# Optimization experiments

Hardware: AMD Instinct MI355X
Metric: run time of the kernel (lower is better)

The kernel has to match this reference:

```python
import jax, jax.numpy as jnp
import numpy as np

B, N, DIM = 8, 1024, 512
HEADS, DIM_HEAD = 8, 64
INNER = HEADS * DIM_HEAD  # 512
SCALE = DIM_HEAD ** -0.5
EPS = 1e-5


def setup_inputs() -> dict:
    key = jax.random.key(0)
    k = jax.random.split(key, 6)
    x = jax.random.normal(k[0], (B, N, DIM), dtype=jnp.float32)
    gamma = jnp.ones((DIM,), dtype=jnp.float32)
    beta = jnp.zeros((DIM,), dtype=jnp.float32)
    # Linear weights stored as (in, out) so y = x @ W (equivalent to torch x @ W.T)
    W_qk = jax.random.normal(k[1], (DIM, 2 * INNER), dtype=jnp.float32) * (DIM ** -0.5)
    W_v = jax.random.normal(k[2], (DIM, INNER), dtype=jnp.float32) * (DIM ** -0.5)
    W_out = jax.random.normal(k[3], (INNER, DIM), dtype=jnp.float32) * (INNER ** -0.5)
    return {"x": x, "gamma": gamma, "beta": beta, "W_qk": W_qk, "W_v": W_v, "W_out": W_out}


def _layernorm(x, gamma, beta):
    mu = jnp.mean(x, axis=-1, keepdims=True)
    var = jnp.mean(jnp.square(x - mu), axis=-1, keepdims=True)
    return (x - mu) * jax.lax.rsqrt(var + EPS) * gamma + beta


def reference(x, gamma, beta, W_qk, W_v, W_out):
    xn = _layernorm(x, gamma, beta)                       # [B,N,D]
    v = xn @ W_v                                          # [B,N,INNER]
    qk = xn @ W_qk                                        # [B,N,2*INNER]
    q, k = jnp.split(qk, 2, axis=-1)
    # b n (h d) -> b h n d
    q = q.reshape(B, N, HEADS, DIM_HEAD).transpose(0, 2, 1, 3)
    k = k.reshape(B, N, HEADS, DIM_HEAD).transpose(0, 2, 1, 3)
    vh = v.reshape(B, N, HEADS, DIM_HEAD).transpose(0, 2, 1, 3)
    dots = jnp.einsum('bhnd,bhmd->bhnm', q, k) * SCALE    # [B,H,N,N]
    attn = jax.nn.softmax(dots, axis=-1)
    out = jnp.einsum('bhnm,bhmd->bhnd', attn, vh)         # [B,H,N,d]
    out = out.transpose(0, 2, 1, 3).reshape(B, N, INNER)  # b h n d -> b n (h d)
    return out @ W_out                                    # [B,N,DIM]
```

## Files before the change

### kernel.cpp

```cpp
#include <hip/hip_runtime.h>

#define TOK 8192
#define DMODEL 512
#define SEQ 1024
#define NH 8
#define DH 64

typedef _Float16 half8 __attribute__((ext_vector_type(8)));
typedef _Float16 half4v __attribute__((ext_vector_type(4)));
typedef float floatx4 __attribute__((ext_vector_type(4)));
typedef unsigned int uint2v __attribute__((ext_vector_type(2)));

__device__ __forceinline__ void gll16(const void* g, void* l) {
  __builtin_amdgcn_global_load_lds(
      (const __attribute__((address_space(1))) void*)g,
      (__attribute__((address_space(3))) void*)l, 16, 0, 0);
}

__device__ __forceinline__ unsigned pk16(float a, float b) {
  auto v = __builtin_amdgcn_cvt_pkrtz(a, b);
  return __builtin_bit_cast(unsigned, v);
}

__global__ __launch_bounds__(256) void prep_kernel(
    const float* __restrict__ x, const float* __restrict__ gamma,
    const float* __restrict__ beta, _Float16* __restrict__ xn,
    const float* __restrict__ Wqk, const float* __restrict__ Wv,
    const float* __restrict__ Wo, _Float16* __restrict__ WqkvT,
    _Float16* __restrict__ WoutT) {
  __shared__ float t[32][33];
  const int bid = blockIdx.x;
  if (bid < 2048) {
    const int row = bid * 4 + (threadIdx.x >> 6);
    const int tt = threadIdx.x & 63;
    const float* xr = x + (size_t)row * DMODEL;
    const float4 a = *(const float4*)(xr + tt * 4);
    const float4 b = *(const float4*)(xr + 256 + tt * 4);
    float s  = a.x + a.y + a.z + a.w + b.x + b.y + b.z + b.w;
    float ss = a.x*a.x + a.y*a.y + a.z*a.z + a.w*a.w
             + b.x*b.x + b.y*b.y + b.z*b.z + b.w*b.w;
    #pragma unroll
    for (int m = 1; m < 64; m <<= 1) {
      s  += __shfl_xor(s, m);
      ss += __shfl_xor(ss, m);
    }
    const float mean = s * (1.0f / DMODEL);
    const float var  = ss * (1.0f / DMODEL) - mean * mean;
    const float inv  = rsqrtf(var + 1e-5f);
    const float4 g0  = *(const float4*)(gamma + tt * 4);
    const float4 g1  = *(const float4*)(gamma + 256 + tt * 4);
    const float4 be0 = *(const float4*)(beta + tt * 4);
    const float4 be1 = *(const float4*)(beta + 256 + tt * 4);
    half4v o0, o1;
    o0[0] = (_Float16)((a.x - mean) * inv * g0.x + be0.x);
    o0[1] = (_Float16)((a.y - mean) * inv * g0.y + be0.y);
    o0[2] = (_Float16)((a.z - mean) * inv * g0.z + be0.z);
    o0[3] = (_Float16)((a.w - mean) * inv * g0.w + be0.w);
    o1[0] = (_Float16)((b.x - mean) * inv * g1.x + be1.x);
    o1[1] = (_Float16)((b.y - mean) * inv * g1.y + be1.y);
    o1[2] = (_Float16)((b.z - mean) * inv * g1.z + be1.z);
    o1[3] = (_Float16)((b.w - mean) * inv * g1.w + be1.w);
    _Float16* outr = xn + (size_t)row * DMODEL;
    *(half4v*)(outr + tt * 4) = o0;
    *(half4v*)(outr + 256 + tt * 4) = o1;
  } else {
    const int r = bid - 2048;
    const int z = r >> 9;
    const int rem = r & 511;
    const float* W;
    _Float16* dst;
    int N, rowoff;
    if (z == 0)      { W = Wqk; dst = WqkvT; N = 1024; rowoff = 0; }
    else if (z == 1) { W = Wv;  dst = WqkvT; N = 512;  rowoff = 1024; }
    else             { W = Wo;  dst = WoutT; N = 512;  rowoff = 0; }
    const int n0 = (rem & 31) * 32;
    if (n0 >= N) return;
    const int k0 = (rem >> 5) * 32;
    const int tx = threadIdx.x & 31, ty = threadIdx.x >> 5;
    #pragma unroll
    for (int j = 0; j < 4; ++j)
      t[ty + j * 8][tx] = W[(size_t)(k0 + ty + j * 8) * N + n0 + tx];
    __syncthreads();
    #pragma unroll
    for (int j = 0; j < 4; ++j)
      dst[(size_t)(rowoff + n0 + ty + j * 8) * 512 + k0 + tx] =
          (_Float16)t[tx][ty + j * 8];
  }
}

__global__ __launch_bounds__(256) void hgemm_qkv(
    const _Float16* __restrict__ A, const _Float16* __restrict__ Bt,
    _Float16* __restrict__ Q, _Float16* __restrict__ V, int K) {
  __shared__ char smem[49152];
  const int tid = threadIdx.x;
  const int bm = blockIdx.x, bn = blockIdx.y;
  const int wv = tid >> 6, lane = tid & 63;
  const int l15 = lane & 15, g = lane >> 4;
  const int wr = wv >> 1, wc = wv & 1;
  const _Float16* Ab = A + (size_t)(bm * 128) * K;
  const _Float16* Bb = Bt + (size_t)(bn * 128) * K;
  const int lrow = lane >> 2;
  const int lchk = (lane & 3) * 16;
  const int ssw = lchk ^ (((lrow >> 1) & 3) << 4);

  #define HG_STAGE(buf, kt)                                                   \
    _Pragma("unroll")                                                         \
    for (int i = 0; i < 2; ++i) {                                             \
      const int rbase = wv * 16 + i * 64;                                     \
      gll16((const char*)(Ab + (size_t)(rbase + lrow) * K + (kt)) + ssw,      \
            smem + (buf) * 16384 + rbase * 64);                               \
      gll16((const char*)(Bb + (size_t)(rbase + lrow) * K + (kt)) + ssw,      \
            smem + (buf) * 16384 + 8192 + rbase * 64);                        \
    }

  floatx4 acc[4][4] = {};
  HG_STAGE(0, 0);
  HG_STAGE(1, 32);
  int cur = 0;
  const int nit = K >> 5;
  for (int it = 0; it < nit; ++it) {
    if (it < nit - 2) asm volatile("s_waitcnt vmcnt(4)" ::: "memory");
    else              asm volatile("s_waitcnt vmcnt(0)" ::: "memory");
    __builtin_amdgcn_s_barrier();
    asm volatile("" ::: "memory");
    const int nxt = cur + 2 >= 3 ? cur - 1 : cur + 2;
    if (it + 2 < nit) { HG_STAGE(nxt, (it + 2) * 32); }
    const char* sb = smem + cur * 16384;
    half8 af[4], bf[4];
    #pragma unroll
    for (int mt = 0; mt < 4; ++mt) {
      const int row = wr * 64 + mt * 16 + l15;
      af[mt] = *(const half8*)(sb + row * 64 +
                               ((g * 16) ^ (((row >> 1) & 3) << 4)));
    }
    #pragma unroll
    for (int nt = 0; nt < 4; ++nt) {
      const int row = wc * 64 + nt * 16 + l15;
      bf[nt] = *(const half8*)(sb + 8192 + row * 64 +
                               ((g * 16) ^ (((row >> 1) & 3) << 4)));
    }
    __builtin_amdgcn_s_setprio(1);
    #pragma unroll
    for (int mt = 0; mt < 4; ++mt)
      #pragma unroll
      for (int nt = 0; nt < 4; ++nt)
        acc[mt][nt] = __builtin_amdgcn_mfma_f32_16x16x32_f16(
            af[mt], bf[nt], acc[mt][nt], 0, 0, 0);
    __builtin_amdgcn_s_setprio(0);
    cur = cur + 1 >= 3 ? 0 : cur + 1;
  }
  #undef HG_STAGE
  const int m0 = bm * 128 + wr * 64;
  const int n0 = bn * 128 + wc * 64;
  #pragma unroll
  for (int mt = 0; mt < 4; ++mt) {
    const int mrow = m0 + mt * 16 + 4 * g;
    const int b = mrow >> 10, tok = mrow & 1023;
    #pragma unroll
    for (int nt = 0; nt < 4; ++nt) {
      const int n = n0 + nt * 16 + l15;
      if (n < 1024) {
        #pragma unroll
        for (int r = 0; r < 4; ++r)
          Q[(size_t)(mrow + r) * 1024 + n] = (_Float16)acc[mt][nt][r];
      } else {
        const int cv = n - 1024;
        half4v hv;
        #pragma unroll
        for (int r = 0; r < 4; ++r) hv[r] = (_Float16)acc[mt][nt][r];
        *(half4v*)(V + ((size_t)((b * 8 + (cv >> 6)) * 64 + (cv & 63)) << 10) + tok) = hv;
      }
    }
  }
}

__global__ __launch_bounds__(512) void hgemm_out(
    const _Float16* __restrict__ A, const _Float16* __restrict__ Bt,
    float* __restrict__ C) {
  __shared__ char smem[49152];
  const int tid = threadIdx.x;
  const int bm = blockIdx.x, bn = blockIdx.y;
  const int wv = tid >> 6, lane = tid & 63;
  const int l15 = lane & 15, g = lane >> 4;
  const int wr = wv >> 2, wc = wv & 3;
  const _Float16* Ab = A + (size_t)(bm * 128) * 512;
  const _Float16* Bb = Bt + (size_t)(bn * 128) * 512;
  const int lrow = lane >> 2;
  const int lchk = (lane & 3) * 16;
  const int ssw = lchk ^ (((lrow >> 1) & 3) << 4);

  #define OUT_STAGE(buf, kt)                                                  \
    {                                                                         \
      gll16((const char*)(Ab + (size_t)(wv * 16 + lrow) * 512 + (kt)) + ssw,  \
            smem + (buf) * 16384 + wv * 16 * 64);                             \
      gll16((const char*)(Bb + (size_t)(wv * 16 + lrow) * 512 + (kt)) + ssw,  \
            smem + (buf) * 16384 + 8192 + wv * 16 * 64);                      \
    }

  floatx4 acc[4][2] = {};
  OUT_STAGE(0, 0);
  OUT_STAGE(1, 32);
  int cur = 0;
  for (int it = 0; it < 16; ++it) {
    if (it < 14) asm volatile("s_waitcnt vmcnt(2)" ::: "memory");
    else         asm volatile("s_waitcnt vmcnt(0)" ::: "memory");
    __builtin_amdgcn_s_barrier();
    asm volatile("" ::: "memory");
    const int nxt = cur + 2 >= 3 ? cur - 1 : cur + 2;
    if (it + 2 < 16) { OUT_STAGE(nxt, (it + 2) * 32); }
    const char* sb = smem + cur * 16384;
    half8 af[4], bf[2];
    #pragma unroll
    for (int mt = 0; mt < 4; ++mt) {
      const int row = wr * 64 + mt * 16 + l15;
      af[mt] = *(const half8*)(sb + row * 64 +
                               ((g * 16) ^ (((row >> 1) & 3) << 4)));
    }
    #pragma unroll
    for (int nt = 0; nt < 2; ++nt) {
      const int row = wc * 32 + nt * 16 + l15;
      bf[nt] = *(const half8*)(sb + 8192 + row * 64 +
                               ((g * 16) ^ (((row >> 1) & 3) << 4)));
    }
    __builtin_amdgcn_s_setprio(1);
    #pragma unroll
    for (int mt = 0; mt < 4; ++mt)
      #pragma unroll
      for (int nt = 0; nt < 2; ++nt)
        acc[mt][nt] = __builtin_amdgcn_mfma_f32_16x16x32_f16(
            af[mt], bf[nt], acc[mt][nt], 0, 0, 0);
    __builtin_amdgcn_s_setprio(0);
    cur = cur + 1 >= 3 ? 0 : cur + 1;
  }
  #undef OUT_STAGE
  const int m0 = bm * 128 + wr * 64;
  const int n0 = bn * 128 + wc * 32;
  #pragma unroll
  for (int mt = 0; mt < 4; ++mt)
    #pragma unroll
    for (int nt = 0; nt < 2; ++nt) {
      const int n = n0 + nt * 16 + l15;
      #pragma unroll
      for (int r = 0; r < 4; ++r)
        C[(size_t)(m0 + mt * 16 + 4 * g + r) * 512 + n] = acc[mt][nt][r];
    }
}

#define QSC 0.18033688f
#define MOFF 5.7707801f

__global__ __launch_bounds__(512) void flash16_kernel(
    const _Float16* __restrict__ qkh, const _Float16* __restrict__ vt,
    _Float16* __restrict__ ao) {
  __shared__ char smem[65536];
  const int bh = blockIdx.x;
  const int qt = blockIdx.y;
  const int b = bh >> 3, h = bh & 7;
  const int tid = threadIdx.x;
  const int wv = tid >> 6, lane = tid & 63;
  const int l15 = lane & 15, g = lane >> 4;
  const int swz = (l15 & 7) << 4;
  const int qrow0 = b * SEQ + qt * 128;

  half8 qf[2];
  {
    const _Float16* qp = qkh + (size_t)(qrow0 + wv * 16 + l15) * 1024 + h * DH;
    qf[0] = *(const half8*)(qp + g * 8);
    qf[1] = *(const half8*)(qp + g * 8 + 32);
    qf[0] *= (_Float16)QSC;
    qf[1] *= (_Float16)QSC;
  }

  float lsum = 0.f;
  floatx4 oacc[4] = {};
  floatx4 minit;
  minit[0] = -MOFF; minit[1] = -MOFF; minit[2] = -MOFF; minit[3] = -MOFF;

  const int lrow = lane >> 3;
  const int lchk = (lane & 7) * 16;
  const int ssw = lchk ^ (lrow << 4);
  const _Float16* kbase = qkh + 512 + h * DH;
  const _Float16* vbase = vt + (size_t)bh * 64 * 1024;
  char* pb = smem + 49152 + wv * 2048 + l15 * 128;

  #define FL_STAGE(buf, kt)                                                   \
    {                                                                         \
      const int krow = b * SEQ + (kt) * 64 + wv * 8 + lrow;                   \
      gll16((const char*)(kbase + (size_t)krow * 1024) + ssw,                 \
            smem + (buf) * 16384 + wv * 1024);                                \
      gll16((const char*)(vbase + (size_t)(wv * 8 + lrow) * 1024 +            \
                          (kt) * 64) + ssw,                                   \
            smem + (buf) * 16384 + 8192 + wv * 1024);                         \
    }

  FL_STAGE(0, 0);
  FL_STAGE(1, 1);
  int cur = 0;
  for (int kt = 0; kt < 16; ++kt) {
    if (kt < 15) asm volatile("s_waitcnt vmcnt(2)" ::: "memory");
    else         asm volatile("s_waitcnt vmcnt(0)" ::: "memory");
    __builtin_amdgcn_s_barrier();
    asm volatile("" ::: "memory");
    const int nxt = cur + 2 >= 3 ? cur - 1 : cur + 2;
    if (kt + 2 < 16) FL_STAGE(nxt, kt + 2);
    const char* sb = smem + cur * 16384;

    floatx4 sacc[4];
    #pragma unroll
    for (int mt = 0; mt < 4; ++mt) sacc[mt] = minit;
    __builtin_amdgcn_s_setprio(1);
    #pragma unroll
    for (int kk = 0; kk < 2; ++kk) {
      #pragma unroll
      for (int mt = 0; mt < 4; ++mt) {
        half8 af = *(const half8*)(sb + (16 * mt + l15) * 128 +
                                   ((g * 16 + kk * 64) ^ swz));
        sacc[mt] = __builtin_amdgcn_mfma_f32_16x16x32_f16(af, qf[kk], sacc[mt], 0, 0, 0);
      }
    }
    __builtin_amdgcn_s_setprio(0);

    float rsp[4];
    #pragma unroll
    for (int mt = 0; mt < 4; ++mt) {
      float p0 = exp2f(sacc[mt][0]);
      float p1 = exp2f(sacc[mt][1]);
      float p2 = exp2f(sacc[mt][2]);
      float p3 = exp2f(sacc[mt][3]);
      rsp[mt] = (p0 + p1) + (p2 + p3);
      uint2v u;
      u[0] = pk16(p0, p1);
      u[1] = pk16(p2, p3);
      *(uint2v*)(pb + ((32 * mt + 8 * g) ^ swz)) = u;
    }
    lsum += (rsp[0] + rsp[1]) + (rsp[2] + rsp[3]);

    __builtin_amdgcn_s_setprio(1);
    #pragma unroll
    for (int kk = 0; kk < 2; ++kk) {
      half8 pf = *(const half8*)(pb + ((g * 16 + kk * 64) ^ swz));
      #pragma unroll
      for (int mt = 0; mt < 4; ++mt) {
        half8 vf = *(const half8*)(sb + 8192 + (16 * mt + l15) * 128 +
                                   ((g * 16 + kk * 64) ^ swz));
        oacc[mt] = __builtin_amdgcn_mfma_f32_16x16x32_f16(vf, pf, oacc[mt], 0, 0, 0);
      }
    }
    __builtin_amdgcn_s_setprio(0);
    cur = cur + 1 >= 3 ? 0 : cur + 1;
  }
  #undef FL_STAGE

  lsum += __shfl_xor(lsum, 16);
  lsum += __shfl_xor(lsum, 32);

  const float inv = 1.0f / lsum;
  _Float16* op = ao + (size_t)(qrow0 + wv * 16 + l15) * 512 + h * DH;
  #pragma unroll
  for (int mt = 0; mt < 4; ++mt) {
    half4v hv;
    hv[0] = (_Float16)(oacc[mt][0] * inv);
    hv[1] = (_Float16)(oacc[mt][1] * inv);
    hv[2] = (_Float16)(oacc[mt][2] * inv);
    hv[3] = (_Float16)(oacc[mt][3] * inv);
    *(half4v*)(op + 16 * mt + 4 * g) = hv;
  }
}

extern "C" void kernel_launch(void* const* d_in, const int* in_sizes, int n_in,
                              void* d_out, int out_size, void* d_ws, size_t ws_size,
                              hipStream_t stream) {
  const float* x     = (const float*)d_in[0];
  const float* gamma = (const float*)d_in[1];
  const float* beta  = (const float*)d_in[2];
  const float* W_qk  = (const float*)d_in[3];
  const float* W_v   = (const float*)d_in[4];
  const float* W_out = (const float*)d_in[5];
  float* out = (float*)d_out;
  char* ws = (char*)d_ws;

  const size_t MB = 1024 * 1024;
  _Float16* xn16  = (_Float16*)ws;
  _Float16* qkh   = (_Float16*)(ws + 8 * MB);
  _Float16* vt    = (_Float16*)(ws + 24 * MB);
  _Float16* ao16  = (_Float16*)(ws + 32 * MB);
  _Float16* WqkvT = (_Float16*)(ws + 40 * MB);
  _Float16* WoutT = (_Float16*)(ws + 42 * MB);

  prep_kernel<<<3584, 256, 0, stream>>>(x, gamma, beta, xn16,
                                        W_qk, W_v, W_out, WqkvT, WoutT);
  hgemm_qkv<<<dim3(64, 12), 256, 0, stream>>>(xn16, WqkvT, qkh, vt, 512);
  flash16_kernel<<<dim3(64, 8), 512, 0, stream>>>(qkh, vt, ao16);
  hgemm_out<<<dim3(64, 4), 512, 0, stream>>>(ao16, WoutT, out);
}
```

Baseline: 72.40 us.

## Process two K/V tiles per iteration with four-buffer double-pair staging

```diff
diff --git a/kernel.cpp b/kernel.cpp
--- a/kernel.cpp
+++ b/kernel.cpp
@@ -252,7 +252,7 @@
 __global__ __launch_bounds__(512) void flash16_kernel(
     const _Float16* __restrict__ qkh, const _Float16* __restrict__ vt,
     _Float16* __restrict__ ao) {
-  __shared__ char smem[65536];
+  __shared__ char smem[81920];
   const int bh = blockIdx.x;
   const int qt = blockIdx.y;
   const int b = bh >> 3, h = bh & 7;
@@ -281,7 +281,7 @@
   const int ssw = lchk ^ (lrow << 4);
   const _Float16* kbase = qkh + 512 + h * DH;
   const _Float16* vbase = vt + (size_t)bh * 64 * 1024;
-  char* pb = smem + 49152 + wv * 2048 + l15 * 128;
+  char* pb = smem + 65536 + wv * 2048 + l15 * 128;
 
   #define FL_STAGE(buf, kt)                                                   \
     {                                                                         \
@@ -293,63 +293,78 @@
             smem + (buf) * 16384 + 8192 + wv * 1024);                         \
     }
 
+  #define FL_TAIL(sb, sacc)                                                   \
+    {                                                                         \
+      float rsp[4];                                                           \
+      _Pragma("unroll")                                                       \
+      for (int mt = 0; mt < 4; ++mt) {                                        \
+        float p0 = exp2f(sacc[mt][0]);                                        \
+        float p1 = exp2f(sacc[mt][1]);                                        \
+        float p2 = exp2f(sacc[mt][2]);                                        \
+        float p3 = exp2f(sacc[mt][3]);                                        \
+        rsp[mt] = (p0 + p1) + (p2 + p3);                                      \
+        uint2v u;                                                             \
+        u[0] = pk16(p0, p1);                                                  \
+        u[1] = pk16(p2, p3);                                                  \
+        *(uint2v*)(pb + ((32 * mt + 8 * g) ^ swz)) = u;                       \
+      }                                                                       \
+      lsum += (rsp[0] + rsp[1]) + (rsp[2] + rsp[3]);                          \
+      __builtin_amdgcn_s_setprio(1);                                          \
+      _Pragma("unroll")                                                       \
+      for (int kk = 0; kk < 2; ++kk) {                                        \
+        half8 pf = *(const half8*)(pb + ((g * 16 + kk * 64) ^ swz));          \
+        _Pragma("unroll")                                                     \
+        for (int mt = 0; mt < 4; ++mt) {                                      \
+          half8 vf = *(const half8*)((sb) + 8192 + (16 * mt + l15) * 128 +    \
+                                     ((g * 16 + kk * 64) ^ swz));             \
+          oacc[mt] = __builtin_amdgcn_mfma_f32_16x16x32_f16(vf, pf,           \
+                                                            oacc[mt], 0, 0, 0);\
+        }                                                                     \
+      }                                                                       \
+      __builtin_amdgcn_s_setprio(0);                                          \
+    }
+
   FL_STAGE(0, 0);
   FL_STAGE(1, 1);
-  int cur = 0;
-  for (int kt = 0; kt < 16; ++kt) {
-    if (kt < 15) asm volatile("s_waitcnt vmcnt(2)" ::: "memory");
-    else         asm volatile("s_waitcnt vmcnt(0)" ::: "memory");
+  for (int p = 0; p < 8; ++p) {
+    asm volatile("s_waitcnt vmcnt(0)" ::: "memory");
     __builtin_amdgcn_s_barrier();
     asm volatile("" ::: "memory");
-    const int nxt = cur + 2 >= 3 ? cur - 1 : cur + 2;
-    if (kt + 2 < 16) FL_STAGE(nxt, kt + 2);
-    const char* sb = smem + cur * 16384;
-
-    floatx4 sacc[4];
-    #pragma unroll
-    for (int mt = 0; mt < 4; ++mt) sacc[mt] = minit;
+    const int b0 = (p & 1) * 2, b1 = b0 + 1;
+    if (p < 7) {
+      FL_STAGE(b0 ^ 2, 2 * p + 2);
+      FL_STAGE(b1 ^ 2, 2 * p + 3);
+    }
+    const char* sb0 = smem + b0 * 16384;
+    const char* sb1 = smem + b1 * 16384;
+
+    floatx4 sacc0[4], sacc1[4];
+    #pragma unroll
+    for (int mt = 0; mt < 4; ++mt) { sacc0[mt] = minit; sacc1[mt] = minit; }
     __builtin_amdgcn_s_setprio(1);
     #pragma unroll
-    for (int kk = 0; kk < 2; ++kk) {
+    for (int kk = 0; kk < 2; ++kk)
       #pragma unroll
       for (int mt = 0; mt < 4; ++mt) {
-        half8 af = *(const half8*)(sb + (16 * mt + l15) * 128 +
+        half8 af = *(const half8*)(sb0 + (16 * mt + l15) * 128 +
                                    ((g * 16 + kk * 64) ^ swz));
-        sacc[mt] = __builtin_amdgcn_mfma_f32_16x16x32_f16(af, qf[kk], sacc[mt], 0, 0, 0);
+        sacc0[mt] = __builtin_amdgcn_mfma_f32_16x16x32_f16(af, qf[kk], sacc0[mt], 0, 0, 0);
       }
-    }
-    __builtin_amdgcn_s_setprio(0);
-
-    float rsp[4];
-    #pragma unroll
-    for (int mt = 0; mt < 4; ++mt) {
-      float p0 = exp2f(sacc[mt][0]);
-      float p1 = exp2f(sacc[mt][1]);
-      float p2 = exp2f(sacc[mt][2]);
-      float p3 = exp2f(sacc[mt][3]);
-      rsp[mt] = (p0 + p1) + (p2 + p3);
-      uint2v u;
-      u[0] = pk16(p0, p1);
-      u[1] = pk16(p2, p3);
-      *(uint2v*)(pb + ((32 * mt + 8 * g) ^ swz)) = u;
-    }
-    lsum += (rsp[0] + rsp[1]) + (rsp[2] + rsp[3]);
-
-    __builtin_amdgcn_s_setprio(1);
-    #pragma unroll
-    for (int kk = 0; kk < 2; ++kk) {
-      half8 pf = *(const half8*)(pb + ((g * 16 + kk * 64) ^ swz));
+    #pragma unroll
+    for (int kk = 0; kk < 2; ++kk)
       #pragma unroll
       for (int mt = 0; mt < 4; ++mt) {
-        half8 vf = *(const half8*)(sb + 8192 + (16 * mt + l15) * 128 +
+        half8 af = *(const half8*)(sb1 + (16 * mt + l15) * 128 +
                                    ((g * 16 + kk * 64) ^ swz));
-        oacc[mt] = __builtin_amdgcn_mfma_f32_16x16x32_f16(vf, pf, oacc[mt], 0, 0, 0);
+        sacc1[mt] = __builtin_amdgcn_mfma_f32_16x16x32_f16(af, qf[kk], sacc1[mt], 0, 0, 0);
       }
-    }
     __builtin_amdgcn_s_setprio(0);
-    cur = cur + 1 >= 3 ? 0 : cur + 1;
+
+    FL_TAIL(sb0, sacc0);
+    FL_TAIL(sb1, sacc1);
   }
   #undef FL_STAGE
+  #undef FL_TAIL
 
   lsum += __shfl_xor(lsum, 16);
   lsum += __shfl_xor(lsum, 32);
```

After: 73.07 us. About the same (+0.9%).
